# Performance work log

Hardware: AMD Instinct MI355X
Metric: run time of the kernel (lower is better)

## Reference

```python
import jax, jax.numpy as jnp
import numpy as np

EPS = 1e-5

def _conv1x1(x, w, b):
    # x: [B,C,H,W], w: [O,C], b: [O]  (1x1 conv == channel matmul)
    return jnp.einsum('bchw,oc->bohw', x, w) + b[None, :, None, None]

def _bn_relu(y, gamma, beta, mean, var):
    inv = gamma / jnp.sqrt(var + EPS)
    return jax.nn.relu(y * inv[None, :, None, None] + (beta - mean * inv)[None, :, None, None])

def setup_inputs() -> dict:
    key = jax.random.key(0)
    ks = jax.random.split(key, 8)
    B, C, H, W = 8, 2048, 48, 48
    mid = C // 4  # k = 4 -> mid_ch = 512
    s_in = (2.0 / C) ** 0.5   # kaiming-like scale for 1x1 convs from C channels
    s_mid = (2.0 / mid) ** 0.5
    return {
        'x': jax.random.normal(ks[0], (B, C, H, W), jnp.float32),
        'f_w': jax.random.normal(ks[1], (mid, C), jnp.float32) * s_in,
        'f_b': jnp.zeros((mid,), jnp.float32),
        'f_gamma': jnp.ones((mid,), jnp.float32),
        'f_beta': jnp.zeros((mid,), jnp.float32),
        'f_mean': jnp.zeros((mid,), jnp.float32),
        'f_var': jnp.ones((mid,), jnp.float32),
        'g_w': jax.random.normal(ks[2], (mid, C), jnp.float32) * s_in,
        'g_b': jnp.zeros((mid,), jnp.float32),
        'g_gamma': jnp.ones((mid,), jnp.float32),
        'g_beta': jnp.zeros((mid,), jnp.float32),
        'g_mean': jnp.zeros((mid,), jnp.float32),
        'g_var': jnp.ones((mid,), jnp.float32),
        'h_w': jax.random.normal(ks[3], (mid, C), jnp.float32) * s_in,
        'h_b': jnp.zeros((mid,), jnp.float32),
        'v_w': jax.random.normal(ks[4], (C, mid), jnp.float32) * s_mid,
        'v_b': jnp.zeros((C,), jnp.float32),
    }

def reference(x, f_w, f_b, f_gamma, f_beta, f_mean, f_var,
              g_w, g_b, g_gamma, g_beta, g_mean, g_var,
              h_w, h_b, v_w, v_b):
    B, C, H, W = x.shape
    mid = f_w.shape[0]
    N = H * W
    f_x = _bn_relu(_conv1x1(x, f_w, f_b), f_gamma, f_beta, f_mean, f_var).reshape(B, mid, N)
    g_x = _bn_relu(_conv1x1(x, g_w, g_b), g_gamma, g_beta, g_mean, g_var).reshape(B, mid, N)
    h_x = _conv1x1(x, h_w, h_b).reshape(B, mid, N)
    # z = f_x^T @ g_x : [B, N, N]
    scores = jnp.einsum('bcn,bcm->bnm', f_x, g_x) * (mid ** -0.5)
    attn = jax.nn.softmax(scores, axis=-1)
    # z = attn @ h_x^T : [B, N, mid] -> [B, mid, H, W]
    z = jnp.einsum('bnm,bcm->bcn', attn, h_x).reshape(B, mid, H, W)
    z = jnp.einsum('bchw,oc->bohw', z, v_w) + v_b[None, :, None, None]
    return (z + x, attn)
```

## Files before the change

### kernel.cpp

```cpp
#include <hip/hip_runtime.h>
#include <math.h>

typedef unsigned short u16;
typedef unsigned short u16x4 __attribute__((ext_vector_type(4)));
typedef unsigned short u16x8 __attribute__((ext_vector_type(8)));
typedef __bf16 bf16x8 __attribute__((ext_vector_type(8)));
typedef float f32x4 __attribute__((ext_vector_type(4)));

typedef __attribute__((address_space(1))) const unsigned int gu32;
typedef __attribute__((address_space(3))) unsigned int su32;

#define B_ 8
#define C_ 2048
#define MID_ 512
#define N_ 2304

static __device__ __forceinline__ u16 f2bf(float f) {
  union { float f; unsigned u; } c; c.f = f;
  unsigned u = c.u;
  u += 0x7fffu + ((u >> 16) & 1u);
  return (u16)(u >> 16);
}

__global__ __launch_bounds__(256) void prep_wall_k(
    const float* __restrict__ fw, const float* __restrict__ gw,
    const float* __restrict__ hw, u16* __restrict__ wall) {
  int idx = blockIdx.x * 256 + threadIdx.x;
  if (idx >= 1536 * 2048) return;
  int r = idx >> 11;
  float v = (r < 512) ? fw[idx] : (r < 1024) ? gw[idx - (512 << 11)] : hw[idx - (1024 << 11)];
  wall[idx] = f2bf(v);
}

__global__ __launch_bounds__(256) void prep_vw_k(const float* __restrict__ vw, u16* __restrict__ o) {
  int idx = blockIdx.x * 256 + threadIdx.x;
  if (idx < 2048 * 512) o[idx] = f2bf(vw[idx]);
}

__global__ __launch_bounds__(256) void prep_sb_k(
    const float* fb, const float* fg, const float* fbe, const float* fm, const float* fv,
    const float* gb, const float* gg, const float* gbe, const float* gm, const float* gv,
    const float* hb, float* __restrict__ scale, float* __restrict__ bias) {
  int i = blockIdx.x * 256 + threadIdx.x;
  if (i >= 1536) return;
  if (i < 512) {
    float inv = fg[i] / sqrtf(fv[i] + 1e-5f);
    scale[i] = inv; bias[i] = fb[i] * inv + fbe[i] - fm[i] * inv;
  } else if (i < 1024) {
    int j = i - 512;
    float inv = gg[j] / sqrtf(gv[j] + 1e-5f);
    scale[i] = inv; bias[i] = gb[j] * inv + gbe[j] - gm[j] * inv;
  } else {
    scale[i] = 1.0f; bias[i] = hb[i - 1024];
  }
}

__global__ __launch_bounds__(256) void transpose_x_k(const float* __restrict__ x, u16* __restrict__ xT) {
  __shared__ float tile[64][68];
  const int b = blockIdx.z;
  const int n0 = blockIdx.x * 64, c0 = blockIdx.y * 64;
  const float* xb = x + (size_t)b * C_ * N_;
  u16* xTb = xT + (size_t)b * N_ * C_;
  const int r = threadIdx.x >> 2, q = threadIdx.x & 3;
  #pragma unroll
  for (int j = 0; j < 4; ++j) {
    float4 v = *(const float4*)&xb[(size_t)(c0 + r) * N_ + n0 + (q + 4 * j) * 4];
    *(float4*)&tile[r][(q + 4 * j) * 4] = v;
  }
  __syncthreads();
  #pragma unroll
  for (int g = 0; g < 2; ++g) {
    const int cl = (q * 2 + g) * 8;
    u16x8 w;
    #pragma unroll
    for (int e = 0; e < 8; ++e) w[e] = f2bf(tile[cl + e][r]);
    *(u16x8*)&xTb[(size_t)(n0 + r) * C_ + c0 + cl] = w;
  }
}

__global__ __launch_bounds__(256) void transpose_h_k(const u16* __restrict__ fghT, u16* __restrict__ hx) {
  __shared__ u16 tile[32][33];
  const int b = blockIdx.z;
  const int n0 = blockIdx.x * 32, c0 = blockIdx.y * 32;
  const u16* src = fghT + (size_t)b * N_ * 1536;
  u16* dst = hx + (size_t)b * MID_ * N_;
  const int tx = threadIdx.x & 31, ty = threadIdx.x >> 5;
  #pragma unroll
  for (int i = 0; i < 4; ++i)
    tile[ty + i * 8][tx] = src[(size_t)(n0 + ty + i * 8) * 1536 + 1024 + c0 + tx];
  __syncthreads();
  #pragma unroll
  for (int i = 0; i < 4; ++i)
    dst[(size_t)(c0 + ty + i * 8) * N_ + n0 + tx] = tile[tx][ty + i * 8];
}

#define EP_FG 0
#define EP_SCORE 2
#define EP_BF16 3
#define EP_FINAL 4

template<int EPI>
__global__ __launch_bounds__(512, 2) void gemm3_kernel(
    const u16* __restrict__ Ag, int lda, long long sA,
    const u16* __restrict__ Bg, int ldb, long long sB,
    void* __restrict__ Cg, int ldc, long long sC, int K,
    const float* __restrict__ ep_scale, const float* __restrict__ ep_bias,
    const float* __restrict__ ep_x, long long sX, float fscale)
{
  extern __shared__ __align__(16) u16 smem[];
  u16* As = smem;
  u16* Bs = smem + 4 * 256 * 32;

  const int tid = threadIdx.x;
  const int lane = tid & 63;
  const int wv = tid >> 6;
  const int b = blockIdx.z;
  const int m0 = blockIdx.y * 256;
  const int n0 = blockIdx.x * 256;
  const int wm = (wv >> 2) * 128;
  const int wn = (wv & 3) * 64;
  const int lr = lane & 15, lg = lane >> 4;

  const u16* Ab = Ag + (size_t)b * sA;
  const u16* Bb = Bg + (size_t)b * sB;

  const int nk = K >> 5;

  const int srow = lane >> 2;
  const int sch  = lane & 3;

  const int cA = ((lg ^ (((wm + lr) >> 1) & 3)) * 8);
  const int cB = ((lg ^ (((wn + lr) >> 1) & 3)) * 8);

  f32x4 acc[8][4];
  #pragma unroll
  for (int i = 0; i < 8; ++i)
    #pragma unroll
    for (int j = 0; j < 4; ++j)
      acc[i][j] = f32x4{0.f, 0.f, 0.f, 0.f};

  auto STAGE = [&](int slot, int kt) {
    #pragma unroll
    for (int j = 0; j < 2; ++j) {
      const int rb = j * 128 + wv * 16;
      const int arow = rb + srow;
      {
        const int gch = sch ^ ((arow >> 1) & 3);
        const u16* ga = Ab + (size_t)(m0 + arow) * lda + kt * 32 + gch * 8;
        __builtin_amdgcn_global_load_lds((gu32*)ga, (su32*)(As + (slot * 256 + rb) * 32), 16, 0, 0);
      }
      {
        const int gch = sch ^ ((arow >> 1) & 3);
        const u16* gb = Bb + (size_t)(n0 + arow) * ldb + kt * 32 + gch * 8;
        __builtin_amdgcn_global_load_lds((gu32*)gb, (su32*)(Bs + (slot * 256 + rb) * 32), 16, 0, 0);
      }
    }
  };

  STAGE(0, 0); STAGE(1, 1); STAGE(2, 2);

  for (int kt = 0; kt < nk; ++kt) {
    const int slot = kt & 3;
    if (kt < nk - 2)        asm volatile("s_waitcnt vmcnt(8)" ::: "memory");
    else if (kt == nk - 2)  asm volatile("s_waitcnt vmcnt(4)" ::: "memory");
    else                    asm volatile("s_waitcnt vmcnt(0)" ::: "memory");
    __builtin_amdgcn_s_barrier();

    const u16* Asl = As + slot * (256 * 32);
    const u16* Bsl = Bs + slot * (256 * 32);
    bf16x8 af[8], bf[4];
    #pragma unroll
    for (int mf = 0; mf < 8; ++mf)
      af[mf] = *(const bf16x8*)(Asl + (wm + mf * 16 + lr) * 32 + cA);
    #pragma unroll
    for (int nf = 0; nf < 4; ++nf)
      bf[nf] = *(const bf16x8*)(Bsl + (wn + nf * 16 + lr) * 32 + cB);

    if (kt + 3 < nk) STAGE((kt + 3) & 3, kt + 3);

    __builtin_amdgcn_s_setprio(1);
    #pragma unroll
    for (int mf = 0; mf < 8; ++mf)
      #pragma unroll
      for (int nf = 0; nf < 4; ++nf)
        acc[mf][nf] = __builtin_amdgcn_mfma_f32_16x16x32_bf16(af[mf], bf[nf], acc[mf][nf], 0, 0, 0);
    __builtin_amdgcn_s_setprio(0);
    asm volatile("s_waitcnt lgkmcnt(0)" ::: "memory");
  }

  u16*   C16 = (u16*)Cg + (size_t)b * sC;
  float* C32 = (float*)Cg + (size_t)b * sC;
  const float* xb = (EPI == EP_FINAL) ? (ep_x + (size_t)b * sX) : nullptr;
  #pragma unroll
  for (int mf = 0; mf < 8; ++mf) {
    #pragma unroll
    for (int nf = 0; nf < 4; ++nf) {
      #pragma unroll
      for (int r = 0; r < 4; ++r) {
        int row = m0 + wm + mf * 16 + lg * 4 + r;
        int col = n0 + wn + nf * 16 + lr;
        float v = acc[mf][nf][r];
        if constexpr (EPI == EP_FG) {
          v = v * ep_scale[col] + ep_bias[col];
          if (col < 1024) v = fmaxf(v, 0.f);
          C16[(size_t)row * ldc + col] = f2bf(v);
        } else if constexpr (EPI == EP_SCORE) {
          C32[(size_t)row * ldc + col] = v * fscale;
        } else if constexpr (EPI == EP_BF16) {
          C16[(size_t)row * ldc + col] = f2bf(v);
        } else {
          v += ep_bias[row] + xb[(size_t)row * ldc + col];
          C32[(size_t)row * ldc + col] = v;
        }
      }
    }
  }
}

__global__ __launch_bounds__(256) void softmax_k(float* __restrict__ attn, u16* __restrict__ P) {
  float* r = attn + (size_t)blockIdx.x * N_;
  u16* pr = P + (size_t)blockIdx.x * N_;
  const int tid = threadIdx.x;
  float4 v0 = *(const float4*)&r[tid * 4];
  float4 v1 = *(const float4*)&r[1024 + tid * 4];
  float  v2 = r[2048 + tid];
  float mx = fmaxf(fmaxf(fmaxf(v0.x, v0.y), fmaxf(v0.z, v0.w)),
                   fmaxf(fmaxf(fmaxf(v1.x, v1.y), fmaxf(v1.z, v1.w)), v2));
  #pragma unroll
  for (int o = 32; o; o >>= 1) mx = fmaxf(mx, __shfl_xor(mx, o));
  __shared__ float red[4], red2[4];
  if ((tid & 63) == 0) red[tid >> 6] = mx;
  __syncthreads();
  mx = fmaxf(fmaxf(red[0], red[1]), fmaxf(red[2], red[3]));
  v0.x = __expf(v0.x - mx); v0.y = __expf(v0.y - mx);
  v0.z = __expf(v0.z - mx); v0.w = __expf(v0.w - mx);
  v1.x = __expf(v1.x - mx); v1.y = __expf(v1.y - mx);
  v1.z = __expf(v1.z - mx); v1.w = __expf(v1.w - mx);
  v2 = __expf(v2 - mx);
  float s = v0.x + v0.y + v0.z + v0.w + v1.x + v1.y + v1.z + v1.w + v2;
  #pragma unroll
  for (int o = 32; o; o >>= 1) s += __shfl_xor(s, o);
  if ((tid & 63) == 0) red2[tid >> 6] = s;
  __syncthreads();
  s = red2[0] + red2[1] + red2[2] + red2[3];
  float inv = 1.0f / s;
  v0.x *= inv; v0.y *= inv; v0.z *= inv; v0.w *= inv;
  v1.x *= inv; v1.y *= inv; v1.z *= inv; v1.w *= inv;
  v2 *= inv;
  *(float4*)&r[tid * 4] = v0;
  *(float4*)&r[1024 + tid * 4] = v1;
  r[2048 + tid] = v2;
  u16x4 p0; p0[0] = f2bf(v0.x); p0[1] = f2bf(v0.y); p0[2] = f2bf(v0.z); p0[3] = f2bf(v0.w);
  u16x4 p1; p1[0] = f2bf(v1.x); p1[1] = f2bf(v1.y); p1[2] = f2bf(v1.z); p1[3] = f2bf(v1.w);
  *(u16x4*)&pr[tid * 4] = p0;
  *(u16x4*)&pr[1024 + tid * 4] = p1;
  pr[2048 + tid] = f2bf(v2);
}

extern "C" void kernel_launch(void* const* d_in, const int* in_sizes, int n_in,
                              void* d_out, int out_size, void* d_ws, size_t ws_size,
                              hipStream_t stream) {
  const float* x    = (const float*)d_in[0];
  const float* f_w  = (const float*)d_in[1];
  const float* f_b  = (const float*)d_in[2];
  const float* f_ga = (const float*)d_in[3];
  const float* f_be = (const float*)d_in[4];
  const float* f_me = (const float*)d_in[5];
  const float* f_va = (const float*)d_in[6];
  const float* g_w  = (const float*)d_in[7];
  const float* g_b  = (const float*)d_in[8];
  const float* g_ga = (const float*)d_in[9];
  const float* g_be = (const float*)d_in[10];
  const float* g_me = (const float*)d_in[11];
  const float* g_va = (const float*)d_in[12];
  const float* h_w  = (const float*)d_in[13];
  const float* h_b  = (const float*)d_in[14];
  const float* v_w  = (const float*)d_in[15];
  const float* v_b  = (const float*)d_in[16];

  float* out0 = (float*)d_out;
  float* attn = out0 + (size_t)B_ * C_ * N_;

  char* p = (char*)d_ws;
  u16* xT   = (u16*)p; p += (size_t)B_ * N_ * C_ * 2;
  u16* fghT = (u16*)p; p += (size_t)B_ * N_ * 1536 * 2;
  u16* hx   = (u16*)p; p += (size_t)B_ * MID_ * N_ * 2;
  u16* ZT   = (u16*)p; p += (size_t)B_ * N_ * MID_ * 2;
  u16* Wall = (u16*)p; p += (size_t)1536 * C_ * 2;
  u16* vwb  = (u16*)p; p += (size_t)C_ * MID_ * 2;
  float* sc = (float*)p; p += 1536 * 4;
  float* bi = (float*)p; p += 1536 * 4;
  u16* P = xT;

  hipFuncSetAttribute((const void*)gemm3_kernel<EP_FG>,    hipFuncAttributeMaxDynamicSharedMemorySize, 131072);
  hipFuncSetAttribute((const void*)gemm3_kernel<EP_SCORE>, hipFuncAttributeMaxDynamicSharedMemorySize, 131072);
  hipFuncSetAttribute((const void*)gemm3_kernel<EP_BF16>,  hipFuncAttributeMaxDynamicSharedMemorySize, 131072);
  hipFuncSetAttribute((const void*)gemm3_kernel<EP_FINAL>, hipFuncAttributeMaxDynamicSharedMemorySize, 131072);

  prep_wall_k<<<(1536 * 2048 + 255) / 256, 256, 0, stream>>>(f_w, g_w, h_w, Wall);
  prep_vw_k<<<(2048 * 512 + 255) / 256, 256, 0, stream>>>(v_w, vwb);
  prep_sb_k<<<6, 256, 0, stream>>>(f_b, f_ga, f_be, f_me, f_va,
                                   g_b, g_ga, g_be, g_me, g_va, h_b, sc, bi);
  transpose_x_k<<<dim3(N_ / 64, C_ / 64, B_), 256, 0, stream>>>(x, xT);

  gemm3_kernel<EP_FG><<<dim3(1536 / 256, N_ / 256, B_), 512, 131072, stream>>>(
      xT, C_, (long long)N_ * C_, Wall, C_, 0,
      fghT, 1536, (long long)N_ * 1536, C_, sc, bi, nullptr, 0, 0.f);

  transpose_h_k<<<dim3(N_ / 32, MID_ / 32, B_), 256, 0, stream>>>(fghT, hx);

  const float fscale = 0.044194173824159216f;
  gemm3_kernel<EP_SCORE><<<dim3(N_ / 256, N_ / 256, B_), 512, 131072, stream>>>(
      fghT, 1536, (long long)N_ * 1536, fghT + 512, 1536, (long long)N_ * 1536,
      attn, N_, (long long)N_ * N_, MID_, nullptr, nullptr, nullptr, 0, fscale);

  softmax_k<<<B_ * N_, 256, 0, stream>>>(attn, P);

  gemm3_kernel<EP_BF16><<<dim3(MID_ / 256, N_ / 256, B_), 512, 131072, stream>>>(
      P, N_, (long long)N_ * N_, hx, N_, (long long)MID_ * N_,
      ZT, MID_, (long long)N_ * MID_, N_, nullptr, nullptr, nullptr, 0, 0.f);

  gemm3_kernel<EP_FINAL><<<dim3(N_ / 256, C_ / 256, B_), 512, 131072, stream>>>(
      vwb, MID_, 0, ZT, MID_, (long long)N_ * MID_,
      out0, N_, (long long)C_ * N_, MID_, nullptr, v_b, x, (long long)C_ * N_, 0.f);
}
```

Baseline: 518.8 us.

## Restructure GEMM to BK=64 double buffer with interleaved MFMA/staging; bf16 score buffer

The GEMM main loop now uses K-tiles of 64 with a two-slot LDS buffer and an XOR swizzle across 8 chunks. Each K-step is split into four MFMA quadrants separated by barriers, with the next tile's B and A global-to-LDS loads issued between quadrants to spread memory traffic through the compute. The score GEMM now writes bf16 scaled scores to a separate workspace instead of fp32 into the attn output. Softmax reads those bf16 scores, writes the fp32 attn output and overwrites the buffer in place with bf16 probabilities, which removes one fp32 read of the large score matrix. Risks include extra barrier overhead and slight precision loss from rounding the pre-softmax scores to bf16.

```diff
diff --git a/kernel.cpp b/kernel.cpp
--- a/kernel.cpp
+++ b/kernel.cpp
@@ -2,7 +2,6 @@
 #include <math.h>
 
 typedef unsigned short u16;
-typedef unsigned short u16x4 __attribute__((ext_vector_type(4)));
 typedef unsigned short u16x8 __attribute__((ext_vector_type(8)));
 typedef __bf16 bf16x8 __attribute__((ext_vector_type(8)));
 typedef float f32x4 __attribute__((ext_vector_type(4)));
@@ -14,12 +13,25 @@
 #define C_ 2048
 #define MID_ 512
 #define N_ 2304
+
+#define BAR() do { asm volatile("" ::: "memory"); __builtin_amdgcn_s_barrier(); asm volatile("" ::: "memory"); } while (0)
+
+#define QMFMA(AV, BV, MO, NO)                                                             \
+  { _Pragma("unroll") for (int mfi = 0; mfi < 4; ++mfi) {                                 \
+      _Pragma("unroll") for (int nfi = 0; nfi < 2; ++nfi) {                               \
+        acc[MO + mfi][NO + nfi] = __builtin_amdgcn_mfma_f32_16x16x32_bf16(                \
+            AV[0][mfi], BV[0][nfi], acc[MO + mfi][NO + nfi], 0, 0, 0);                    \
+        acc[MO + mfi][NO + nfi] = __builtin_amdgcn_mfma_f32_16x16x32_bf16(                \
+            AV[1][mfi], BV[1][nfi], acc[MO + mfi][NO + nfi], 0, 0, 0); } } }
 
 static __device__ __forceinline__ u16 f2bf(float f) {
   union { float f; unsigned u; } c; c.f = f;
   unsigned u = c.u;
   u += 0x7fffu + ((u >> 16) & 1u);
   return (u16)(u >> 16);
+}
+static __device__ __forceinline__ float bf2f(u16 x) {
+  union { unsigned u; float f; } c; c.u = ((unsigned)x) << 16; return c.f;
 }
 
 __global__ __launch_bounds__(256) void prep_wall_k(
@@ -95,12 +107,11 @@
 }
 
 #define EP_FG 0
-#define EP_SCORE 2
-#define EP_BF16 3
-#define EP_FINAL 4
+#define EP_SCALE16 1
+#define EP_FINAL 2
 
 template<int EPI>
-__global__ __launch_bounds__(512, 2) void gemm3_kernel(
+__global__ __launch_bounds__(512, 2) void gemm4_kernel(
     const u16* __restrict__ Ag, int lda, long long sA,
     const u16* __restrict__ Bg, int ldb, long long sB,
     void* __restrict__ Cg, int ldc, long long sC, int K,
@@ -109,7 +120,7 @@
 {
   extern __shared__ __align__(16) u16 smem[];
   u16* As = smem;
-  u16* Bs = smem + 4 * 256 * 32;
+  u16* Bs = smem + 2 * 256 * 64;
 
   const int tid = threadIdx.x;
   const int lane = tid & 63;
@@ -123,14 +134,13 @@
 
   const u16* Ab = Ag + (size_t)b * sA;
   const u16* Bb = Bg + (size_t)b * sB;
-
-  const int nk = K >> 5;
-
-  const int srow = lane >> 2;
-  const int sch  = lane & 3;
-
-  const int cA = ((lg ^ (((wm + lr) >> 1) & 3)) * 8);
-  const int cB = ((lg ^ (((wn + lr) >> 1) & 3)) * 8);
+  const int nk = K >> 6;
+
+  const int srow = lane >> 3;
+  const int sksw = ((lane & 7) ^ srow) * 8;
+
+  const int rdsw0 = ((0 + lg) ^ (lr & 7)) * 8;
+  const int rdsw1 = ((4 + lg) ^ (lr & 7)) * 8;
 
   f32x4 acc[8][4];
   #pragma unroll
@@ -139,53 +149,88 @@
     for (int j = 0; j < 4; ++j)
       acc[i][j] = f32x4{0.f, 0.f, 0.f, 0.f};
 
-  auto STAGE = [&](int slot, int kt) {
-    #pragma unroll
-    for (int j = 0; j < 2; ++j) {
-      const int rb = j * 128 + wv * 16;
-      const int arow = rb + srow;
-      {
-        const int gch = sch ^ ((arow >> 1) & 3);
-        const u16* ga = Ab + (size_t)(m0 + arow) * lda + kt * 32 + gch * 8;
-        __builtin_amdgcn_global_load_lds((gu32*)ga, (su32*)(As + (slot * 256 + rb) * 32), 16, 0, 0);
-      }
-      {
-        const int gch = sch ^ ((arow >> 1) & 3);
-        const u16* gb = Bb + (size_t)(n0 + arow) * ldb + kt * 32 + gch * 8;
-        __builtin_amdgcn_global_load_lds((gu32*)gb, (su32*)(Bs + (slot * 256 + rb) * 32), 16, 0, 0);
-      }
+  auto STAGE_A = [&](int p2, int t) {
+    #pragma unroll
+    for (int j = 0; j < 4; ++j) {
+      const int rb = j * 64 + wv * 8;
+      const u16* g = Ab + (size_t)(m0 + rb + srow) * lda + t * 64 + sksw;
+      __builtin_amdgcn_global_load_lds((gu32*)g, (su32*)(As + p2 * 16384 + rb * 64), 16, 0, 0);
     }
   };
-
-  STAGE(0, 0); STAGE(1, 1); STAGE(2, 2);
+  auto STAGE_B = [&](int p2, int t) {
+    #pragma unroll
+    for (int j = 0; j < 4; ++j) {
+      const int rb = j * 64 + wv * 8;
+      const u16* g = Bb + (size_t)(n0 + rb + srow) * ldb + t * 64 + sksw;
+      __builtin_amdgcn_global_load_lds((gu32*)g, (su32*)(Bs + p2 * 16384 + rb * 64), 16, 0, 0);
+    }
+  };
+
+  STAGE_A(0, 0); STAGE_B(0, 0);
+  if (nk > 1) { STAGE_A(1, 1); STAGE_B(1, 1); }
 
   for (int kt = 0; kt < nk; ++kt) {
-    const int slot = kt & 3;
-    if (kt < nk - 2)        asm volatile("s_waitcnt vmcnt(8)" ::: "memory");
-    else if (kt == nk - 2)  asm volatile("s_waitcnt vmcnt(4)" ::: "memory");
-    else                    asm volatile("s_waitcnt vmcnt(0)" ::: "memory");
-    __builtin_amdgcn_s_barrier();
-
-    const u16* Asl = As + slot * (256 * 32);
-    const u16* Bsl = Bs + slot * (256 * 32);
-    bf16x8 af[8], bf[4];
-    #pragma unroll
-    for (int mf = 0; mf < 8; ++mf)
-      af[mf] = *(const bf16x8*)(Asl + (wm + mf * 16 + lr) * 32 + cA);
-    #pragma unroll
-    for (int nf = 0; nf < 4; ++nf)
-      bf[nf] = *(const bf16x8*)(Bsl + (wn + nf * 16 + lr) * 32 + cB);
-
-    if (kt + 3 < nk) STAGE((kt + 3) & 3, kt + 3);
-
+    const int p = kt & 1;
+    if (kt + 1 < nk) asm volatile("s_waitcnt vmcnt(8)" ::: "memory");
+    else             asm volatile("s_waitcnt vmcnt(0)" ::: "memory");
+    BAR();
+
+    const u16* Asl = As + p * 16384;
+    const u16* Bsl = Bs + p * 16384;
+    const bool st = (kt + 2) < nk;
+    const int ps = (kt + 2) & 1;
+
+    bf16x8 aV[2][4], bLo[2][2], bHi[2][2];
+
+    #pragma unroll
+    for (int ks = 0; ks < 2; ++ks) {
+      const int ro = ks ? rdsw1 : rdsw0;
+      #pragma unroll
+      for (int i = 0; i < 4; ++i)
+        aV[ks][i] = *(const bf16x8*)(Asl + (wm + i * 16 + lr) * 64 + ro);
+      #pragma unroll
+      for (int i = 0; i < 2; ++i)
+        bLo[ks][i] = *(const bf16x8*)(Bsl + (wn + i * 16 + lr) * 64 + ro);
+    }
+    BAR();
     __builtin_amdgcn_s_setprio(1);
-    #pragma unroll
-    for (int mf = 0; mf < 8; ++mf)
-      #pragma unroll
-      for (int nf = 0; nf < 4; ++nf)
-        acc[mf][nf] = __builtin_amdgcn_mfma_f32_16x16x32_bf16(af[mf], bf[nf], acc[mf][nf], 0, 0, 0);
+    QMFMA(aV, bLo, 0, 0);
     __builtin_amdgcn_s_setprio(0);
-    asm volatile("s_waitcnt lgkmcnt(0)" ::: "memory");
+    BAR();
+
+    #pragma unroll
+    for (int ks = 0; ks < 2; ++ks) {
+      const int ro = ks ? rdsw1 : rdsw0;
+      #pragma unroll
+      for (int i = 0; i < 2; ++i)
+        bHi[ks][i] = *(const bf16x8*)(Bsl + (wn + 32 + i * 16 + lr) * 64 + ro);
+    }
+    BAR();
+    __builtin_amdgcn_s_setprio(1);
+    QMFMA(aV, bHi, 0, 2);
+    __builtin_amdgcn_s_setprio(0);
+    BAR();
+
+    #pragma unroll
+    for (int ks = 0; ks < 2; ++ks) {
+      const int ro = ks ? rdsw1 : rdsw0;
+      #pragma unroll
+      for (int i = 0; i < 4; ++i)
+        aV[ks][i] = *(const bf16x8*)(Asl + (wm + 64 + i * 16 + lr) * 64 + ro);
+    }
+    if (st) STAGE_B(ps, kt + 2);
+    BAR();
+    __builtin_amdgcn_s_setprio(1);
+    QMFMA(aV, bLo, 4, 0);
+    __builtin_amdgcn_s_setprio(0);
+    BAR();
+
+    if (st) STAGE_A(ps, kt + 2);
+    BAR();
+    __builtin_amdgcn_s_setprio(1);
+    QMFMA(aV, bHi, 4, 2);
+    __builtin_amdgcn_s_setprio(0);
+    BAR();
   }
 
   u16*   C16 = (u16*)Cg + (size_t)b * sC;
@@ -204,10 +249,8 @@
           v = v * ep_scale[col] + ep_bias[col];
           if (col < 1024) v = fmaxf(v, 0.f);
           C16[(size_t)row * ldc + col] = f2bf(v);
-        } else if constexpr (EPI == EP_SCORE) {
-          C32[(size_t)row * ldc + col] = v * fscale;
-        } else if constexpr (EPI == EP_BF16) {
-          C16[(size_t)row * ldc + col] = f2bf(v);
+        } else if constexpr (EPI == EP_SCALE16) {
+          C16[(size_t)row * ldc + col] = f2bf(v * fscale);
         } else {
           v += ep_bias[row] + xb[(size_t)row * ldc + col];
           C32[(size_t)row * ldc + col] = v;
@@ -217,44 +260,46 @@
   }
 }
 
-__global__ __launch_bounds__(256) void softmax_k(float* __restrict__ attn, u16* __restrict__ P) {
-  float* r = attn + (size_t)blockIdx.x * N_;
-  u16* pr = P + (size_t)blockIdx.x * N_;
+__global__ __launch_bounds__(256) void softmax_k(u16* __restrict__ SP, float* __restrict__ attn) {
+  u16* sp = SP + (size_t)blockIdx.x * N_;
+  float* ar = attn + (size_t)blockIdx.x * N_;
   const int tid = threadIdx.x;
-  float4 v0 = *(const float4*)&r[tid * 4];
-  float4 v1 = *(const float4*)&r[1024 + tid * 4];
-  float  v2 = r[2048 + tid];
-  float mx = fmaxf(fmaxf(fmaxf(v0.x, v0.y), fmaxf(v0.z, v0.w)),
-                   fmaxf(fmaxf(fmaxf(v1.x, v1.y), fmaxf(v1.z, v1.w)), v2));
+  u16x8 s8 = *(const u16x8*)&sp[tid * 8];
+  u16 st = sp[2048 + tid];
+  float w[8], wt = bf2f(st);
+  #pragma unroll
+  for (int j = 0; j < 8; ++j) w[j] = bf2f(s8[j]);
+  float mx = wt;
+  #pragma unroll
+  for (int j = 0; j < 8; ++j) mx = fmaxf(mx, w[j]);
   #pragma unroll
   for (int o = 32; o; o >>= 1) mx = fmaxf(mx, __shfl_xor(mx, o));
   __shared__ float red[4], red2[4];
   if ((tid & 63) == 0) red[tid >> 6] = mx;
   __syncthreads();
   mx = fmaxf(fmaxf(red[0], red[1]), fmaxf(red[2], red[3]));
-  v0.x = __expf(v0.x - mx); v0.y = __expf(v0.y - mx);
-  v0.z = __expf(v0.z - mx); v0.w = __expf(v0.w - mx);
-  v1.x = __expf(v1.x - mx); v1.y = __expf(v1.y - mx);
-  v1.z = __expf(v1.z - mx); v1.w = __expf(v1.w - mx);
-  v2 = __expf(v2 - mx);
-  float s = v0.x + v0.y + v0.z + v0.w + v1.x + v1.y + v1.z + v1.w + v2;
+  float s = 0.f;
+  #pragma unroll
+  for (int j = 0; j < 8; ++j) { w[j] = __expf(w[j] - mx); s += w[j]; }
+  wt = __expf(wt - mx); s += wt;
   #pragma unroll
   for (int o = 32; o; o >>= 1) s += __shfl_xor(s, o);
   if ((tid & 63) == 0) red2[tid >> 6] = s;
   __syncthreads();
   s = red2[0] + red2[1] + red2[2] + red2[3];
   float inv = 1.0f / s;
-  v0.x *= inv; v0.y *= inv; v0.z *= inv; v0.w *= inv;
-  v1.x *= inv; v1.y *= inv; v1.z *= inv; v1.w *= inv;
-  v2 *= inv;
-  *(float4*)&r[tid * 4] = v0;
-  *(float4*)&r[1024 + tid * 4] = v1;
-  r[2048 + tid] = v2;
-  u16x4 p0; p0[0] = f2bf(v0.x); p0[1] = f2bf(v0.y); p0[2] = f2bf(v0.z); p0[3] = f2bf(v0.w);
-  u16x4 p1; p1[0] = f2bf(v1.x); p1[1] = f2bf(v1.y); p1[2] = f2bf(v1.z); p1[3] = f2bf(v1.w);
-  *(u16x4*)&pr[tid * 4] = p0;
-  *(u16x4*)&pr[1024 + tid * 4] = p1;
-  pr[2048 + tid] = f2bf(v2);
+  #pragma unroll
+  for (int j = 0; j < 8; ++j) w[j] *= inv;
+  wt *= inv;
+  float4 o0 = {w[0], w[1], w[2], w[3]}, o1 = {w[4], w[5], w[6], w[7]};
+  *(float4*)&ar[tid * 8] = o0;
+  *(float4*)&ar[tid * 8 + 4] = o1;
+  ar[2048 + tid] = wt;
+  u16x8 p8;
+  #pragma unroll
+  for (int j = 0; j < 8; ++j) p8[j] = f2bf(w[j]);
+  *(u16x8*)&sp[tid * 8] = p8;
+  sp[2048 + tid] = f2bf(wt);
 }
 
 extern "C" void kernel_launch(void* const* d_in, const int* in_sizes, int n_in,
@@ -290,12 +335,11 @@
   u16* vwb  = (u16*)p; p += (size_t)C_ * MID_ * 2;
   float* sc = (float*)p; p += 1536 * 4;
   float* bi = (float*)p; p += 1536 * 4;
-  u16* P = xT;
-
-  hipFuncSetAttribute((const void*)gemm3_kernel<EP_FG>,    hipFuncAttributeMaxDynamicSharedMemorySize, 131072);
-  hipFuncSetAttribute((const void*)gemm3_kernel<EP_SCORE>, hipFuncAttributeMaxDynamicSharedMemorySize, 131072);
-  hipFuncSetAttribute((const void*)gemm3_kernel<EP_BF16>,  hipFuncAttributeMaxDynamicSharedMemorySize, 131072);
-  hipFuncSetAttribute((const void*)gemm3_kernel<EP_FINAL>, hipFuncAttributeMaxDynamicSharedMemorySize, 131072);
+  u16* SP   = (u16*)p; p += (size_t)B_ * N_ * N_ * 2;
+
+  hipFuncSetAttribute((const void*)gemm4_kernel<EP_FG>,      hipFuncAttributeMaxDynamicSharedMemorySize, 131072);
+  hipFuncSetAttribute((const void*)gemm4_kernel<EP_SCALE16>, hipFuncAttributeMaxDynamicSharedMemorySize, 131072);
+  hipFuncSetAttribute((const void*)gemm4_kernel<EP_FINAL>,   hipFuncAttributeMaxDynamicSharedMemorySize, 131072);
 
   prep_wall_k<<<(1536 * 2048 + 255) / 256, 256, 0, stream>>>(f_w, g_w, h_w, Wall);
   prep_vw_k<<<(2048 * 512 + 255) / 256, 256, 0, stream>>>(v_w, vwb);
@@ -303,24 +347,24 @@
                                    g_b, g_ga, g_be, g_me, g_va, h_b, sc, bi);
   transpose_x_k<<<dim3(N_ / 64, C_ / 64, B_), 256, 0, stream>>>(x, xT);
 
-  gemm3_kernel<EP_FG><<<dim3(1536 / 256, N_ / 256, B_), 512, 131072, stream>>>(
+  gemm4_kernel<EP_FG><<<dim3(1536 / 256, N_ / 256, B_), 512, 131072, stream>>>(
       xT, C_, (long long)N_ * C_, Wall, C_, 0,
       fghT, 1536, (long long)N_ * 1536, C_, sc, bi, nullptr, 0, 0.f);
 
   transpose_h_k<<<dim3(N_ / 32, MID_ / 32, B_), 256, 0, stream>>>(fghT, hx);
 
   const float fscale = 0.044194173824159216f;
-  gemm3_kernel<EP_SCORE><<<dim3(N_ / 256, N_ / 256, B_), 512, 131072, stream>>>(
+  gemm4_kernel<EP_SCALE16><<<dim3(N_ / 256, N_ / 256, B_), 512, 131072, stream>>>(
       fghT, 1536, (long long)N_ * 1536, fghT + 512, 1536, (long long)N_ * 1536,
-      attn, N_, (long long)N_ * N_, MID_, nullptr, nullptr, nullptr, 0, fscale);
-
-  softmax_k<<<B_ * N_, 256, 0, stream>>>(attn, P);
-
-  gemm3_kernel<EP_BF16><<<dim3(MID_ / 256, N_ / 256, B_), 512, 131072, stream>>>(
-      P, N_, (long long)N_ * N_, hx, N_, (long long)MID_ * N_,
-      ZT, MID_, (long long)N_ * MID_, N_, nullptr, nullptr, nullptr, 0, 0.f);
-
-  gemm3_kernel<EP_FINAL><<<dim3(N_ / 256, C_ / 256, B_), 512, 131072, stream>>>(
+      SP, N_, (long long)N_ * N_, MID_, nullptr, nullptr, nullptr, 0, fscale);
+
+  softmax_k<<<B_ * N_, 256, 0, stream>>>(SP, attn);
+
+  gemm4_kernel<EP_SCALE16><<<dim3(MID_ / 256, N_ / 256, B_), 512, 131072, stream>>>(
+      SP, N_, (long long)N_ * N_, hx, N_, (long long)MID_ * N_,
+      ZT, MID_, (long long)N_ * MID_, N_, nullptr, nullptr, nullptr, 0, 1.0f);
+
+  gemm4_kernel<EP_FINAL><<<dim3(N_ / 256, C_ / 256, B_), 512, 131072, stream>>>(
       vwb, MID_, 0, ZT, MID_, (long long)N_ * MID_,
       out0, N_, (long long)C_ * N_, MID_, nullptr, v_b, x, (long long)C_ * N_, 0.f);
 }
```

Result: no change. 514.0 us (-0.9%).
